# Optimization experiments

Hardware: AMD Instinct MI355X
Metric: run time of the kernel (lower is better)

## Reference

```python
import jax, jax.numpy as jnp
import numpy as np
from jax import lax

ALPHA = 0.5
KERNEL = 25
NUM_P = 16
SEQ_LEN = 1440
PRED_LEN = 720
DWT_LEN = SEQ_LEN // 2 + 2            # 722 (pytorch_wavelets zero-mode, sym3 filt len 6)
FREQ = int(np.ceil(DWT_LEN / 2 * ALPHA) * 2)  # 362

_DEC_LO = np.array([0.035226291882100656, -0.08544127388224149, -0.13501102001039084,
                    0.4598775021193313, 0.8068915093133388, 0.3326705529509569], np.float32)
_DEC_HI = np.array([-0.3326705529509569, 0.8068915093133388, -0.4598775021193313,
                    -0.13501102001039084, 0.08544127388224149, 0.035226291882100656], np.float32)
DEC_LO, DEC_HI = jnp.asarray(_DEC_LO), jnp.asarray(_DEC_HI)
REC_LO, REC_HI = DEC_LO[::-1], DEC_HI[::-1]


def dwt1(x):
    # pytorch_wavelets DWT1DForward(J=1, mode='zero'): zero-pad then stride-2 true conv with dec filters
    B, C, L = x.shape
    out = (L + 5) // 2
    p = 2 * (out - 1) - L + 6
    xp = jnp.pad(x.reshape(B * C, 1, L), ((0, 0), (0, 0), (p // 2, p - p // 2)))
    ker = jnp.stack([DEC_LO[::-1], DEC_HI[::-1]])[:, None, :]   # (2,1,6); xcorr w/ reversed == conv
    y = lax.conv_general_dilated(xp, ker, (2,), 'VALID', dimension_numbers=('NCH', 'OIH', 'NCH'))
    return y[:, 0].reshape(B, C, out), y[:, 1].reshape(B, C, out)


def iwt1(lo, hi):
    # DWT1DInverse mode='zero': conv_transpose stride 2, padding L-2  ->  dilate + conv, pad 1
    B, C, n = lo.shape
    z = jnp.concatenate([lo.reshape(B * C, 1, n), hi.reshape(B * C, 1, n)], axis=1)
    ker = jnp.stack([REC_LO[::-1], REC_HI[::-1]])[None, :, :]   # (O=1, I=2, 6)
    y = lax.conv_general_dilated(z, ker, (1,), [(1, 1)], lhs_dilation=(2,),
                                 dimension_numbers=('NCH', 'OIH', 'NCH'))
    return y[:, 0].reshape(B, C, 2 * n - 4)


def mov_avg(x, k=KERNEL):
    pooled = lax.reduce_window(x, 0.0, lax.add, (1, 1, k), (1, 1, 1), 'VALID') / k
    return jnp.pad(pooled, ((0, 0), (0, 0), (k // 2, k // 2 - (k + 1) % 2)), mode='edge')


def mov_norm(x):
    mean = lax.stop_gradient(mov_avg(x))
    xc = lax.stop_gradient(x - mean)
    std = lax.stop_gradient(mov_avg(jnp.abs(xc))) + 1e-5
    return xc / std, mean, std


def inst_norm(x):
    mean = lax.stop_gradient(jnp.mean(x, -1, keepdims=True))
    xc = x - mean
    var = jnp.mean((xc - jnp.mean(xc, -1, keepdims=True)) ** 2, -1, keepdims=True)
    return xc / jnp.sqrt(var + 1e-5)


def mean_std_mlp(mean, std, mp, sp, mw1, mw2, sw1, sw2, mpred, spred):
    m_all = jnp.mean(mean, -1, keepdims=True)
    s_all = jnp.mean(std, -1, keepdims=True)
    mr = (mean - m_all) @ mp.T
    sr = (std - s_all) @ sp.T
    mr = jax.nn.relu(mr @ mw1.T) @ mw2.T
    sr = jax.nn.relu(sr @ sw1.T) @ sw2.T
    mean_o = mr @ mpred.T + m_all
    std_o = jax.nn.relu(sr @ spred.T + s_all) + 1e-5
    return mean_o, std_o


def forward(x, latent_w, latent_b, acp, dcp):
    xt = jnp.swapaxes(x, -1, 1)                    # (B, C, L)
    ac0, dc0 = dwt1(xt)                            # (B, C, DWT_LEN)
    ac_n = inst_norm(ac0)
    ac, m_ac, s_ac = mov_norm(ac0)
    dc, m_dc, s_dc = mov_norm(dc0)
    m_ac, s_ac = mean_std_mlp(m_ac, s_ac, *acp)    # MLPs[-1]
    m_dc, s_dc = mean_std_mlp(m_dc, s_dc, *dcp)    # MLPs[0]
    dcF = jnp.fft.fft(dc)
    acF = jnp.fft.fft(ac_n)
    idx = jnp.argsort(-jnp.abs(acF), axis=-1)[..., :FREQ]
    amp = ALPHA * jnp.take_along_axis(acF, idx, -1) + (1.0 - ALPHA) * jnp.take_along_axis(dcF, idx, -1)
    B, C, _ = dcF.shape
    bi = jnp.arange(B)[:, None, None]
    ci = jnp.arange(C)[None, :, None]
    dcF = dcF.at[bi, ci, idx].set(amp)
    dc = jnp.real(jnp.fft.ifft(dcF))
    xr = iwt1(ac, dc)                              # (B, C, SEQ_LEN)
    mean = iwt1(m_ac, m_dc)                        # (B, C, PRED_LEN)
    std = iwt1(s_ac, s_dc)
    xr = xr.reshape(B, C, NUM_P, SEQ_LEN // NUM_P)
    emb = xr @ latent_w.T + latent_b               # (B, C, NUM_P, d_model)
    return emb, mean, std


def setup_inputs() -> dict:
    key = jax.random.key(0)
    B, C = 64, 128
    d_model, d_ff = 512, 1024
    s = 0.02
    names_shapes = [
        ('x', (B, SEQ_LEN, C), 1.0),
        ('latent_w', (d_model, SEQ_LEN // NUM_P), s),
    ]
    for pre in ('ac', 'dc'):
        names_shapes += [
            (pre + '_mean_proj', (d_model, DWT_LEN), s),
            (pre + '_std_proj', (d_model, DWT_LEN), s),
            (pre + '_mean_ffn_w1', (d_ff, d_model), s),
            (pre + '_mean_ffn_w2', (d_model, d_ff), s),
            (pre + '_std_ffn_w1', (d_ff, d_model), s),
            (pre + '_std_ffn_w2', (d_model, d_ff), s),
            (pre + '_mean_pred', (PRED_LEN // 2 + 2, d_model), s),
            (pre + '_std_pred', (PRED_LEN // 2 + 2, d_model), s),
        ]
    keys = jax.random.split(key, len(names_shapes))
    inp = {n: jax.random.normal(k, shp, dtype=jnp.float32) * sc
           for (n, shp, sc), k in zip(names_shapes, keys)}
    inp['latent_b'] = jnp.zeros((d_model,), jnp.float32)
    return inp


def reference(x, latent_w, latent_b,
              ac_mean_proj, ac_std_proj, ac_mean_ffn_w1, ac_mean_ffn_w2,
              ac_std_ffn_w1, ac_std_ffn_w2, ac_mean_pred, ac_std_pred,
              dc_mean_proj, dc_std_proj, dc_mean_ffn_w1, dc_mean_ffn_w2,
              dc_std_ffn_w1, dc_std_ffn_w2, dc_mean_pred, dc_std_pred):
    acp = (ac_mean_proj, ac_std_proj, ac_mean_ffn_w1, ac_mean_ffn_w2,
           ac_std_ffn_w1, ac_std_ffn_w2, ac_mean_pred, ac_std_pred)
    dcp = (dc_mean_proj, dc_std_proj, dc_mean_ffn_w1, dc_mean_ffn_w2,
           dc_std_ffn_w1, dc_std_ffn_w2, dc_mean_pred, dc_std_pred)
    return forward(x, latent_w, latent_b, acp, dcp)
```

## Files before the change

kernel.cpp:

```cpp
#include <hip/hip_runtime.h>
#include <cmath>

#define RTOT 8192
#define NDWT 722
#define KP1  736
#define LSEQ 1440
#define NHEAD 362
#define NFREQ 362

typedef __bf16 bf16x8 __attribute__((ext_vector_type(8)));
typedef float f32x4 __attribute__((ext_vector_type(4)));
typedef float f32x2 __attribute__((ext_vector_type(2)));

__device__ __forceinline__ unsigned short f2bf(float f) {
    unsigned u = __float_as_uint(f);
    u += 0x7fffu + ((u >> 16) & 1u);
    return (unsigned short)(u >> 16);
}
__device__ __forceinline__ float bf2f(unsigned short u) {
    return __uint_as_float(((unsigned)u) << 16);
}

__device__ __forceinline__ void cmac(f32x2& s, f32x2 a, f32x2 w) {
    asm("v_pk_fma_f32 %0, %1, %2, %0 op_sel:[0,0,0] op_sel_hi:[0,1,1]\n\t"
        "v_pk_fma_f32 %0, %1, %2, %0 op_sel:[1,1,0] op_sel_hi:[1,0,1] neg_lo:[0,1,0]"
        : "+v"(s) : "v"(a), "v"(w));
}
__device__ __forceinline__ f32x2 cmul(f32x2 a, f32x2 b) {
    f32x2 r;
    asm("v_pk_mul_f32 %0, %1, %2 op_sel:[0,0] op_sel_hi:[0,1]\n\t"
        "v_pk_fma_f32 %0, %1, %2, %0 op_sel:[1,1,0] op_sel_hi:[1,0,1] neg_lo:[0,1,0]"
        : "=&v"(r) : "v"(a), "v"(b));
    return r;
}

__constant__ float c_lo[6] = {0.035226291882100656f, -0.08544127388224149f, -0.13501102001039084f,
                              0.4598775021193313f, 0.8068915093133388f, 0.3326705529509569f};
__constant__ float c_hi[6] = {-0.3326705529509569f, 0.8068915093133388f, -0.4598775021193313f,
                              -0.13501102001039084f, 0.08544127388224149f, 0.035226291882100656f};

__global__ void wtab_kernel(float2* __restrict__ Wtab) {
    int m = blockIdx.x * blockDim.x + threadIdx.x;
    if (m < NDWT) {
        double ang = -2.0 * 3.141592653589793238462643383279502884 * (double)m / (double)NDWT;
        Wtab[m] = make_float2((float)cos(ang), (float)sin(ang));
    }
}

struct CvtDesc { const float* src; unsigned short* dst; int N, K, Np, Kp; };
struct CvtArgs { CvtDesc d[17]; };
__global__ __launch_bounds__(256) void cvt_all_kernel(CvtArgs a) {
    CvtDesc d = a.d[blockIdx.y];
    int idx = blockIdx.x * 256 + threadIdx.x;
    int tot = d.Np * d.Kp;
    if (idx >= tot) return;
    int r = idx / d.Kp, c = idx - r * d.Kp;
    float v = (r < d.N && c < d.K) ? d.src[(size_t)r * d.K + c] : 0.f;
    d.dst[idx] = f2bf(v);
}

__global__ __launch_bounds__(512) void dwt_kernel(const float* __restrict__ x,
                                                  float* __restrict__ ac0,
                                                  float* __restrict__ dc0) {
    int b = blockIdx.x;
    int c = threadIdx.x;
    int t0 = blockIdx.y * 16 + threadIdx.y * 4;
    for (int i = 0; i < 4; i++) {
        int t = t0 + i;
        if (t >= NDWT) break;
        float slo = 0.f, shi = 0.f;
        #pragma unroll
        for (int j = 0; j < 6; j++) {
            int l = 2 * t + 1 - j;
            float v = (l >= 0 && l < LSEQ) ? x[((size_t)b * LSEQ + l) * 128 + c] : 0.f;
            slo += v * c_lo[j];
            shi += v * c_hi[j];
        }
        size_t o = ((size_t)b * 128 + c) * NDWT + t;
        ac0[o] = slo;
        dc0[o] = shi;
    }
}

__device__ __forceinline__ float blockSum256(float v, float* red) {
    #pragma unroll
    for (int o = 32; o > 0; o >>= 1) v += __shfl_down(v, o, 64);
    int lane = threadIdx.x & 63, wid = threadIdx.x >> 6;
    __syncthreads();
    if (lane == 0) red[wid] = v;
    __syncthreads();
    return red[0] + red[1] + red[2] + red[3];
}

template <bool ABS>
__device__ __forceinline__ void pool25(const float* rowv, float* pool, int tid) {
    int i0 = tid * 3;
    if (i0 < 698) {
        float s25 = 0.f;
        #pragma unroll
        for (int j = 0; j < 25; j++) { float v = rowv[i0 + j]; s25 += ABS ? fabsf(v) : v; }
        pool[i0] = s25 * (1.f / 25.f);
        #pragma unroll
        for (int qq = 1; qq < 3; qq++) {
            int i = i0 + qq;
            if (i < 698) {
                float vin = rowv[i + 24], vout = rowv[i - 1];
                s25 += (ABS ? fabsf(vin) : vin) - (ABS ? fabsf(vout) : vout);
                pool[i] = s25 * (1.f / 25.f);
            }
        }
    }
}

__global__ __launch_bounds__(256) void rowstats_kernel(
    const float* __restrict__ ac0in, const float* __restrict__ dc0in,
    float* __restrict__ acn,
    float* __restrict__ acp,
    float* __restrict__ dcp,
    unsigned short* __restrict__ cent,
    float* __restrict__ stat ) {
    __shared__ float row[NDWT];
    __shared__ float xc[NDWT];
    __shared__ float pool[698];
    __shared__ float red[4];
    const int r = blockIdx.x, tid = threadIdx.x;
    const size_t base = (size_t)r * NDWT;
    const size_t baseP = (size_t)r * KP1;
    const size_t CS = (size_t)RTOT * KP1;

    if (blockIdx.y == 0) {
        for (int i = tid; i < NDWT; i += 256) row[i] = ac0in[base + i];
        __syncthreads();
        float s = 0.f;
        for (int i = tid; i < NDWT; i += 256) s += row[i];
        float mean = blockSum256(s, red) * (1.f / 722.f);
        s = 0.f;
        for (int i = tid; i < NDWT; i += 256) s += row[i] - mean;
        float m2 = blockSum256(s, red) * (1.f / 722.f);
        s = 0.f;
        for (int i = tid; i < NDWT; i += 256) { float d = row[i] - mean - m2; s += d * d; }
        float var = blockSum256(s, red) * (1.f / 722.f);
        float inv = 1.f / sqrtf(var + 1e-5f);
        for (int i = tid; i < NDWT; i += 256) acn[base + i] = (row[i] - mean) * inv;

        pool25<false>(row, pool, tid);
        __syncthreads();
        float msum = 0.f;
        for (int l = tid; l < NDWT; l += 256) {
            int pi = l - 12; pi = pi < 0 ? 0 : (pi > 697 ? 697 : pi);
            float m = pool[pi];
            msum += m;
            xc[l] = row[l] - m;
        }
        float m_all = blockSum256(msum, red) * (1.f / 722.f);
        __syncthreads();
        pool25<true>(xc, pool, tid);
        __syncthreads();
        float ssum = 0.f;
        for (int l = tid; l < NDWT; l += 256) {
            int pi = l - 12; pi = pi < 0 ? 0 : (pi > 697 ? 697 : pi);
            float sd = pool[pi] + 1e-5f;
            ssum += sd;
            acp[base + l] = xc[l] / sd;
        }
        float s_all = blockSum256(ssum, red) * (1.f / 722.f);
        if (tid == 0) { stat[r] = m_all; stat[RTOT + r] = s_all; }
        for (int l = tid; l < KP1; l += 256) {
            if (l < NDWT) {
                float m = row[l] - xc[l];
                int pi = l - 12; pi = pi < 0 ? 0 : (pi > 697 ? 697 : pi);
                float sd = pool[pi] + 1e-5f;
                cent[baseP + l]      = f2bf(m - m_all);
                cent[CS + baseP + l] = f2bf(sd - s_all);
            } else { cent[baseP + l] = 0; cent[CS + baseP + l] = 0; }
        }
    } else {
        for (int i = tid; i < NDWT; i += 256) row[i] = dc0in[base + i];
        __syncthreads();
        pool25<false>(row, pool, tid);
        __syncthreads();
        float msum2 = 0.f;
        for (int l = tid; l < NDWT; l += 256) {
            int pi = l - 12; pi = pi < 0 ? 0 : (pi > 697 ? 697 : pi);
            float m = pool[pi];
            msum2 += m;
            xc[l] = row[l] - m;
        }
        float m_all2 = blockSum256(msum2, red) * (1.f / 722.f);
        __syncthreads();
        pool25<true>(xc, pool, tid);
        __syncthreads();
        float ssum2 = 0.f;
        for (int l = tid; l < NDWT; l += 256) {
            int pi = l - 12; pi = pi < 0 ? 0 : (pi > 697 ? 697 : pi);
            float sd = pool[pi] + 1e-5f;
            ssum2 += sd;
            dcp[base + l] = xc[l] / sd;
        }
        float s_all2 = blockSum256(ssum2, red) * (1.f / 722.f);
        if (tid == 0) { stat[2 * RTOT + r] = m_all2; stat[3 * RTOT + r] = s_all2; }
        for (int l = tid; l < KP1; l += 256) {
            if (l < NDWT) {
                float m = row[l] - xc[l];
                int pi = l - 12; pi = pi < 0 ? 0 : (pi > 697 ? 697 : pi);
                float sd = pool[pi] + 1e-5f;
                cent[2 * CS + baseP + l] = f2bf(m - m_all2);
                cent[3 * CS + baseP + l] = f2bf(sd - s_all2);
            } else { cent[2 * CS + baseP + l] = 0; cent[3 * CS + baseP + l] = 0; }
        }
    }
}

__device__ void fft722_dev(f32x2* X, f32x2* T, const f32x2* Wt, const f32x2* W19) {
    const int tid = threadIdx.x;
    if (tid < 190) {
        const int c = tid / 38;
        const int g = tid - c * 38;
        const int p = (g >= 19) ? 1 : 0;
        const int rr = g - 19 * p;
        const int t0 = c * 4;
        const int nt = (c == 4) ? 3 : 4;
        const f32x2* xp = X + 2 * rr + p;
        f32x2 st[4], w[4], s[4];
        #pragma unroll
        for (int i = 0; i < 4; i++) {
            int ti = t0 + i; if (ti > 18) ti = 0;
            st[i] = W19[ti];
            w[i] = f32x2{1.f, 0.f};
            s[i] = f32x2{0.f, 0.f};
        }
        for (int j = 0; j < 19; j++) {
            f32x2 a = xp[38 * j];
            #pragma unroll
            for (int i = 0; i < 4; i++) { cmac(s[i], a, w[i]); w[i] = cmul(w[i], st[i]); }
        }
        f32x2* Tp = T + p * 361 + rr * 19 + t0;
        #pragma unroll
        for (int i = 0; i < 4; i++) if (i < nt) Tp[i] = s[i];
    }
    __syncthreads();
    if (tid < 190) {
        const int c = tid / 38;
        const int g = tid - c * 38;
        const int p = (g >= 19) ? 1 : 0;
        const int t = g - 19 * p;
        const int j0 = c * 4;
        const int nj = (c == 4) ? 3 : 4;
        const f32x2* Tp = T + p * 361 + t;
        int kk[4];
        f32x2 st[4], w[4], s[4];
        #pragma unroll
        for (int i = 0; i < 4; i++) {
            int jj = j0 + i;
            kk[i] = (jj > 18) ? 0 : (t + 19 * jj);
            st[i] = Wt[2 * kk[i]];
            w[i] = f32x2{1.f, 0.f};
            s[i] = f32x2{0.f, 0.f};
        }
        for (int rr = 0; rr < 19; rr++) {
            f32x2 a = Tp[19 * rr];
            #pragma unroll
            for (int i = 0; i < 4; i++) { cmac(s[i], a, w[i]); w[i] = cmul(w[i], st[i]); }
        }
        f32x2* Xp = X + p * 361;
        #pragma unroll
        for (int i = 0; i < 4; i++) if (i < nj) Xp[kk[i]] = s[i];
    }
    __syncthreads();
    for (int k = tid; k < 361; k += 256) {
        f32x2 e = X[k], o = X[361 + k], w = Wt[k];
        f32x2 tt = {0.f, 0.f};
        cmac(tt, o, w);
        X[k] = e + tt;
        X[361 + k] = e - tt;
    }
    __syncthreads();
}

__global__ __launch_bounds__(256) void fft_mix_kernel(const float* __restrict__ acn,
                                                      float* __restrict__ dcp,
                                                      const f32x2* __restrict__ Wtab) {
    __shared__ f32x2 Wt[NDWT];
    __shared__ f32x2 W19s[19];
    __shared__ f32x2 B1[NDWT];
    __shared__ f32x2 B2[NDWT];
    __shared__ float smag[NDWT];
    __shared__ unsigned hist[256];
    __shared__ unsigned suf[256];
    __shared__ unsigned sh_digit, sh_rem;
    const int r = blockIdx.x, tid = threadIdx.x;
    const size_t base = (size_t)r * NDWT;

    for (int i = tid; i < NDWT; i += 256) Wt[i] = Wtab[i];
    if (tid < 19) W19s[tid] = Wtab[38 * tid];
    for (int i = tid; i < NDWT; i += 256) B1[i] = f32x2{acn[base + i], dcp[base + i]};
    __syncthreads();
    fft722_dev(B1, B2, Wt, W19s);
    for (int k = tid; k < 362; k += 256) {
        int m = (NDWT - k) % NDWT;
        f32x2 zk = B1[k], zm = B1[m];
        f32x2 ak = {0.5f * (zk.x + zm.x), 0.5f * (zk.y - zm.y)};
        f32x2 dk = {0.5f * (zk.y + zm.y), 0.5f * (zm.x - zk.x)};
        B1[k] = ak; B2[k] = dk;
        smag[k] = ak.x * ak.x + ak.y * ak.y;
        if (m != k) {
            f32x2 am = {0.5f * (zm.x + zk.x), 0.5f * (zm.y - zk.y)};
            f32x2 dm = {0.5f * (zm.y + zk.y), 0.5f * (zk.x - zm.x)};
            B1[m] = am; B2[m] = dm;
            smag[m] = am.x * am.x + am.y * am.y;
        }
    }
    __syncthreads();

    unsigned prefix = 0, rem = NFREQ;
    for (int shift = 24; shift >= 0; shift -= 8) {
        hist[tid] = 0;
        __syncthreads();
        unsigned hm = (shift == 24) ? 0u : (0xFFFFFFFFu << (shift + 8));
        for (int i = tid; i < NDWT; i += 256) {
            unsigned b = __float_as_uint(smag[i]);
            if ((b & hm) == prefix) atomicAdd(&hist[(b >> shift) & 255], 1u);
        }
        __syncthreads();
        suf[tid] = hist[tid];
        __syncthreads();
        for (int off = 1; off < 256; off <<= 1) {
            unsigned v = (tid + off < 256) ? suf[tid + off] : 0;
            __syncthreads();
            suf[tid] += v;
            __syncthreads();
        }
        unsigned Shere = suf[tid];
        unsigned Snext = (tid < 255) ? suf[tid + 1] : 0;
        if (Shere >= rem && Snext < rem) { sh_digit = (unsigned)tid; sh_rem = rem - Snext; }
        __syncthreads();
        prefix |= (sh_digit << shift);
        rem = sh_rem;
        __syncthreads();
    }
    int c0 = tid * 3, cnt = 0;
    #pragma unroll
    for (int j = 0; j < 3; j++) {
        int i = c0 + j;
        if (i < NDWT && __float_as_uint(smag[i]) == prefix) cnt++;
    }
    suf[tid] = (unsigned)cnt;
    __syncthreads();
    for (int off = 1; off < 256; off <<= 1) {
        unsigned v = (tid >= off) ? suf[tid - off] : 0;
        __syncthreads();
        suf[tid] += v;
        __syncthreads();
    }
    int myexc = (int)suf[tid] - cnt, o = 0;
    #pragma unroll
    for (int j = 0; j < 3; j++) {
        int i = c0 + j;
        if (i < NDWT) {
            unsigned b = __float_as_uint(smag[i]);
            int f = (b > prefix) ? 1 : 0;
            if (b == prefix) { if ((unsigned)(myexc + o) < rem) f = 1; o++; }
            smag[i] = f ? 1.f : 0.f;
        }
    }
    __syncthreads();

    for (int i = tid; i < NDWT; i += 256) {
        f32x2 d = B2[i];
        if (smag[i] != 0.f) { f32x2 a = B1[i]; d.x = 0.5f * (a.x + d.x); d.y = 0.5f * (a.y + d.y); }
        B1[i] = f32x2{d.x, -d.y};
    }
    __syncthreads();
    fft722_dev(B1, B2, Wt, W19s);
    for (int i = tid; i < NDWT; i += 256) dcp[base + i] = B1[i].x * (1.f / 722.f);
}

__global__ __launch_bounds__(256) void iwt_heads_kernel(const unsigned short* __restrict__ heads,
                                                        float* __restrict__ out_mean,
                                                        float* __restrict__ out_std) {
    const int z = blockIdx.z;
    const int r = blockIdx.x;
    const int t = blockIdx.y * 256 + threadIdx.x;
    if (t >= 720) return;
    const size_t HR = (size_t)RTOT * NHEAD;
    const unsigned short* lp = heads + (size_t)z * HR + (size_t)r * NHEAD;
    const unsigned short* hp = heads + (size_t)(2 + z) * HR + (size_t)r * NHEAD;
    float* out = (z ? out_std : out_mean) + (size_t)r * 720;
    float s = 0.f;
    if (t & 1) {
        int j0 = (t - 1) >> 1;
        #pragma unroll
        for (int i = 0; i < 3; i++) s += bf2f(lp[j0 + i]) * c_lo[2 * i] + bf2f(hp[j0 + i]) * c_hi[2 * i];
    } else {
        int j0 = t >> 1;
        #pragma unroll
        for (int i = 0; i < 3; i++) s += bf2f(lp[j0 + i]) * c_lo[2 * i + 1] + bf2f(hp[j0 + i]) * c_hi[2 * i + 1];
    }
    out[t] = s;
}

__global__ __launch_bounds__(256) void iwt_xr_kernel(const float* __restrict__ lo,
                                                     const float* __restrict__ hi,
                                                     unsigned short* __restrict__ xrbf) {
    const int r = blockIdx.x;
    const int t = blockIdx.y * 256 + threadIdx.x;
    if (blockIdx.y == 0 && threadIdx.x < 96) {
        int sub = threadIdx.x / 6, c = 90 + threadIdx.x % 6;
        xrbf[((size_t)r * 16 + sub) * 96 + c] = 0;
    }
    if (t >= LSEQ) return;
    const float* lp = lo + (size_t)r * NDWT;
    const float* hp = hi + (size_t)r * NDWT;
    float s = 0.f;
    if (t & 1) {
        int j0 = (t - 1) >> 1;
        #pragma unroll
        for (int i = 0; i < 3; i++) s += lp[j0 + i] * c_lo[2 * i] + hp[j0 + i] * c_hi[2 * i];
    } else {
        int j0 = t >> 1;
        #pragma unroll
        for (int i = 0; i < 3; i++) s += lp[j0 + i] * c_lo[2 * i + 1] + hp[j0 + i] * c_hi[2 * i + 1];
    }
    xrbf[((size_t)r * 16 + t / 90) * 96 + (t % 90)] = f2bf(s);
}

struct ZPtrs { const unsigned short* p[4]; };
template <int EPI>
__global__ __launch_bounds__(256) void mfma_gemm_z(
    const unsigned short* __restrict__ A, int lda, size_t zsA,
    ZPtrs Wz, int ldw,
    void* __restrict__ Cout, int ldc, size_t zsC, int Nc,
    const float* __restrict__ biasBase, const float* __restrict__ cbias,
    int Ksteps) {
    __shared__ unsigned short As[2][128 * 32];
    __shared__ unsigned short Bs[2][128 * 32];
    const int z = blockIdx.z;
    const unsigned short* Az = A + (size_t)z * zsA;
    const unsigned short* W = Wz.p[z];
    const int tid = threadIdx.x;
    const int lane = tid & 63, wid = tid >> 6;
    const int bm = blockIdx.x * 128, bn = blockIdx.y * 128;
    const int wr = (wid >> 1) * 64, wc = (wid & 1) * 64;
    f32x4 acc[4][4] = {};
    const int srow = (lane >> 2);
    const int scol = (lane & 3) * 8;
    const int ch0 = wid * 2, ch1 = wid * 2 + 1;
    const unsigned short* ga0 = Az + (size_t)(bm + ch0 * 16 + srow) * lda + scol;
    const unsigned short* ga1 = Az + (size_t)(bm + ch1 * 16 + srow) * lda + scol;
    const unsigned short* gb0 = W + (size_t)(bn + ch0 * 16 + srow) * ldw + scol;
    const unsigned short* gb1 = W + (size_t)(bn + ch1 * 16 + srow) * ldw + scol;

#define STAGE_GL(buf, ks) do { const int k0_ = (ks) * 32;                                      \
    __builtin_amdgcn_global_load_lds((const __attribute__((address_space(1))) unsigned int*)(ga0 + k0_), \
        (__attribute__((address_space(3))) unsigned int*)(&As[buf][ch0 * 512]), 16, 0, 0);     \
    __builtin_amdgcn_global_load_lds((const __attribute__((address_space(1))) unsigned int*)(gb0 + k0_), \
        (__attribute__((address_space(3))) unsigned int*)(&Bs[buf][ch0 * 512]), 16, 0, 0);     \
    __builtin_amdgcn_global_load_lds((const __attribute__((address_space(1))) unsigned int*)(ga1 + k0_), \
        (__attribute__((address_space(3))) unsigned int*)(&As[buf][ch1 * 512]), 16, 0, 0);     \
    __builtin_amdgcn_global_load_lds((const __attribute__((address_space(1))) unsigned int*)(gb1 + k0_), \
        (__attribute__((address_space(3))) unsigned int*)(&Bs[buf][ch1 * 512]), 16, 0, 0);     \
    } while (0)

    STAGE_GL(0, 0);
    __syncthreads();
    int cur = 0;
    const int kof = (lane >> 4) * 8;
    for (int ks = 0; ks < Ksteps; ks++) {
        if (ks + 1 < Ksteps) STAGE_GL(cur ^ 1, ks + 1);
        bf16x8 af[4], bfr[4];
        #pragma unroll
        for (int m = 0; m < 4; m++)
            af[m] = *reinterpret_cast<const bf16x8*>(&As[cur][(wr + m * 16 + (lane & 15)) * 32 + kof]);
        #pragma unroll
        for (int n = 0; n < 4; n++)
            bfr[n] = *reinterpret_cast<const bf16x8*>(&Bs[cur][(wc + n * 16 + (lane & 15)) * 32 + kof]);
        #pragma unroll
        for (int m = 0; m < 4; m++)
            #pragma unroll
            for (int n = 0; n < 4; n++)
                acc[m][n] = __builtin_amdgcn_mfma_f32_16x16x32_bf16(af[m], bfr[n], acc[m][n], 0, 0, 0);
        __syncthreads();
        cur ^= 1;
    }
#undef STAGE_GL

    unsigned short* Cb = (unsigned short*)Cout + (size_t)z * zsC;
    float* Cf = (float*)Cout + (size_t)z * zsC;
    const int crow0 = bm + wr + (lane >> 4) * 4;
    const int ccol0 = bn + wc + (lane & 15);
    #pragma unroll
    for (int m = 0; m < 4; m++) {
        #pragma unroll
        for (int n = 0; n < 4; n++) {
            const int col = ccol0 + n * 16;
            if (col < Nc) {
                #pragma unroll
                for (int q = 0; q < 4; q++) {
                    const int row = crow0 + m * 16 + q;
                    float v = acc[m][n][q];
                    if (EPI == 0) {
                        Cb[(size_t)row * ldc + col] = f2bf(v);
                    } else if (EPI == 1) {
                        Cb[(size_t)row * ldc + col] = f2bf(fmaxf(v, 0.f));
                    } else if (EPI == 4) {
                        Cf[(size_t)row * ldc + col] = v + cbias[col];
                    } else {
                        float ob = biasBase[(size_t)z * RTOT + row];
                        if (z & 1) v = fmaxf(v + ob, 0.f) + 1e-5f;
                        else       v += ob;
                        Cb[(size_t)row * ldc + col] = f2bf(v);
                    }
                }
            }
        }
    }
}

extern "C" void kernel_launch(void* const* d_in, const int* in_sizes, int n_in,
                              void* d_out, int out_size, void* d_ws, size_t ws_size,
                              hipStream_t stream) {
    const float* x = (const float*)d_in[0];
    const float* latent_w = (const float*)d_in[1];
    int p0;
    const float* latent_b;
    if (n_in > 2 && in_sizes[2] == 512) { latent_b = (const float*)d_in[2]; p0 = 3; }
    else                                { latent_b = (const float*)d_in[18]; p0 = 2; }

    char* wp = (char*)d_ws;
    auto alloc = [&](size_t bytes) { char* p = wp; wp += (bytes + 255) & ~(size_t)255; return p; };
    const size_t RN = (size_t)RTOT * NDWT;
    float* acn  = (float*)alloc(RN * 4);
    float* dcb  = (float*)alloc(RN * 4);
    float* acp  = (float*)alloc(RN * 4);
    float* stat = (float*)alloc(4 * RTOT * 4);
    float2* Wtab = (float2*)alloc(NDWT * 8);
    unsigned short* cent  = (unsigned short*)alloc((size_t)4 * RTOT * KP1 * 2);
    unsigned short* mlpB4 = (unsigned short*)alloc((size_t)4 * RTOT * 512 * 2);
    unsigned short* mlpA4 = (unsigned short*)alloc((size_t)4 * RTOT * 1024 * 2);
    unsigned short* mlpC4 = (unsigned short*)alloc((size_t)4 * RTOT * 512 * 2);
    unsigned short* heads = mlpB4;
    unsigned short* xrbf = mlpC4;
    unsigned short *projW[4], *w1W[4], *w2W[4], *predW[4];
    for (int z = 0; z < 4; z++) {
        projW[z] = (unsigned short*)alloc((size_t)512 * KP1 * 2);
        w1W[z]   = (unsigned short*)alloc((size_t)1024 * 512 * 2);
        w2W[z]   = (unsigned short*)alloc((size_t)512 * 1024 * 2);
        predW[z] = (unsigned short*)alloc((size_t)384 * 512 * 2);
    }
    unsigned short* latwb = (unsigned short*)alloc((size_t)512 * 96 * 2);
    (void)ws_size;

    CvtArgs ca;
    int si = 0;
    for (int z = 0; z < 4; z++) {
        int branch = z >> 1, isStd = z & 1, wb = p0 + branch * 8;
        ca.d[si++] = {(const float*)d_in[wb + isStd],         projW[z], 512, NDWT, 512, KP1};
        ca.d[si++] = {(const float*)d_in[wb + 2 + 2 * isStd], w1W[z], 1024, 512, 1024, 512};
        ca.d[si++] = {(const float*)d_in[wb + 3 + 2 * isStd], w2W[z], 512, 1024, 512, 1024};
        ca.d[si++] = {(const float*)d_in[wb + 6 + isStd],     predW[z], NHEAD, 512, 384, 512};
    }
    ca.d[16] = {latent_w, latwb, 512, 90, 512, 96};
    cvt_all_kernel<<<dim3(2048, 17), dim3(256), 0, stream>>>(ca);

    wtab_kernel<<<dim3(3), dim3(256), 0, stream>>>(Wtab);
    dwt_kernel<<<dim3(64, 46), dim3(128, 4), 0, stream>>>(x, acn, dcb);
    rowstats_kernel<<<dim3(RTOT, 2), dim3(256), 0, stream>>>(acn, dcb, acn, acp, dcb, cent, stat);
    fft_mix_kernel<<<dim3(RTOT), dim3(256), 0, stream>>>(acn, dcb, (const f32x2*)Wtab);

    ZPtrs Zp = {{projW[0], projW[1], projW[2], projW[3]}};
    ZPtrs Z1 = {{w1W[0], w1W[1], w1W[2], w1W[3]}};
    ZPtrs Z2 = {{w2W[0], w2W[1], w2W[2], w2W[3]}};
    ZPtrs Zh = {{predW[0], predW[1], predW[2], predW[3]}};
    mfma_gemm_z<0><<<dim3(64, 4, 4), dim3(256), 0, stream>>>(
        cent, KP1, (size_t)RTOT * KP1, Zp, KP1, mlpB4, 512, (size_t)RTOT * 512, 512, nullptr, nullptr, KP1 / 32);
    mfma_gemm_z<1><<<dim3(64, 8, 4), dim3(256), 0, stream>>>(
        mlpB4, 512, (size_t)RTOT * 512, Z1, 512, mlpA4, 1024, (size_t)RTOT * 1024, 1024, nullptr, nullptr, 16);
    mfma_gemm_z<0><<<dim3(64, 4, 4), dim3(256), 0, stream>>>(
        mlpA4, 1024, (size_t)RTOT * 1024, Z2, 1024, mlpC4, 512, (size_t)RTOT * 512, 512, nullptr, nullptr, 32);
    mfma_gemm_z<5><<<dim3(64, 3, 4), dim3(256), 0, stream>>>(
        mlpC4, 512, (size_t)RTOT * 512, Zh, 512, heads, NHEAD, (size_t)RTOT * NHEAD, NHEAD, stat, nullptr, 16);

    float* out = (float*)d_out;
    float* out_mean = out + (size_t)67108864;
    float* out_std  = out_mean + (size_t)5898240;
    iwt_heads_kernel<<<dim3(RTOT, 3, 2), dim3(256), 0, stream>>>(heads, out_mean, out_std);
    iwt_xr_kernel<<<dim3(RTOT, 6), dim3(256), 0, stream>>>(acp, dcb, xrbf);

    ZPtrs Zl = {{latwb, latwb, latwb, latwb}};
    mfma_gemm_z<4><<<dim3(1024, 4, 1), dim3(256), 0, stream>>>(
        xrbf, 96, 0, Zl, 96, out, 512, 0, 512, nullptr, latent_b, 3);
}
```

Before: 615.9 us.

## Tile DWT through LDS for coalesced stores; use explicit vmcnt waits in GEMM loop

The DWT kernel now stages a 68x128 input tile in shared memory using float4 loads. Each thread then computes along time for a fixed channel, so the writes into the channel-major (b,c,t) outputs are coalesced along t, where before they were strided. The GEMM main loop replaces __syncthreads with explicit s_waitcnt vmcnt counters plus raw s_barrier, so the next stage's global-to-LDS loads can stay in flight while the current tile is consumed. The hand-written waitcnt logic depends on the exact count of outstanding loads per stage (four), and getting it wrong would be a correctness risk.

```diff
diff --git a/kernel.cpp b/kernel.cpp
--- a/kernel.cpp
+++ b/kernel.cpp
@@ -59,26 +59,42 @@
     d.dst[idx] = f2bf(v);
 }
 
-__global__ __launch_bounds__(512) void dwt_kernel(const float* __restrict__ x,
+__global__ __launch_bounds__(256) void dwt_kernel(const float* __restrict__ x,
                                                   float* __restrict__ ac0,
                                                   float* __restrict__ dc0) {
-    int b = blockIdx.x;
-    int c = threadIdx.x;
-    int t0 = blockIdx.y * 16 + threadIdx.y * 4;
-    for (int i = 0; i < 4; i++) {
-        int t = t0 + i;
-        if (t >= NDWT) break;
-        float slo = 0.f, shi = 0.f;
-        #pragma unroll
-        for (int j = 0; j < 6; j++) {
-            int l = 2 * t + 1 - j;
-            float v = (l >= 0 && l < LSEQ) ? x[((size_t)b * LSEQ + l) * 128 + c] : 0.f;
-            slo += v * c_lo[j];
-            shi += v * c_hi[j];
-        }
-        size_t o = ((size_t)b * 128 + c) * NDWT + t;
-        ac0[o] = slo;
-        dc0[o] = shi;
+    __shared__ float xs[68][129];
+    const int b = blockIdx.x;
+    const int t0 = blockIdx.y * 32;
+    const int tid = threadIdx.x;
+    const int lbase = 2 * t0 - 4;
+    for (int i = tid; i < 68 * 32; i += 256) {
+        int ri = i >> 5;
+        int c4 = (i & 31) * 4;
+        int l = lbase + ri;
+        float4 v = make_float4(0.f, 0.f, 0.f, 0.f);
+        if (l >= 0 && l < LSEQ)
+            v = *reinterpret_cast<const float4*>(&x[((size_t)b * LSEQ + l) * 128 + c4]);
+        xs[ri][c4] = v.x; xs[ri][c4 + 1] = v.y; xs[ri][c4 + 2] = v.z; xs[ri][c4 + 3] = v.w;
+    }
+    __syncthreads();
+    const int tt = tid & 31;
+    const int t = t0 + tt;
+    const int cw = tid >> 5;
+    if (t < NDWT) {
+        #pragma unroll 4
+        for (int co = 0; co < 16; co++) {
+            int c = co * 8 + cw;
+            float slo = 0.f, shi = 0.f;
+            #pragma unroll
+            for (int j = 0; j < 6; j++) {
+                float v = xs[2 * tt + 5 - j][c];
+                slo += v * c_lo[j];
+                shi += v * c_hi[j];
+            }
+            size_t o = ((size_t)b * 128 + c) * NDWT + t;
+            ac0[o] = slo;
+            dc0[o] = shi;
+        }
     }
 }
 
@@ -462,11 +478,17 @@
     } while (0)
 
     STAGE_GL(0, 0);
-    __syncthreads();
     int cur = 0;
     const int kof = (lane >> 4) * 8;
     for (int ks = 0; ks < Ksteps; ks++) {
-        if (ks + 1 < Ksteps) STAGE_GL(cur ^ 1, ks + 1);
+        if (ks + 1 < Ksteps) {
+            STAGE_GL(cur ^ 1, ks + 1);
+            asm volatile("s_waitcnt vmcnt(4)" ::: "memory");
+        } else {
+            asm volatile("s_waitcnt vmcnt(0)" ::: "memory");
+        }
+        __builtin_amdgcn_s_barrier();
+        __builtin_amdgcn_sched_barrier(0);
         bf16x8 af[4], bfr[4];
         #pragma unroll
         for (int m = 0; m < 4; m++)
@@ -479,7 +501,8 @@
             #pragma unroll
             for (int n = 0; n < 4; n++)
                 acc[m][n] = __builtin_amdgcn_mfma_f32_16x16x32_bf16(af[m], bfr[n], acc[m][n], 0, 0, 0);
-        __syncthreads();
+        __builtin_amdgcn_s_barrier();
+        __builtin_amdgcn_sched_barrier(0);
         cur ^= 1;
     }
 #undef STAGE_GL
@@ -563,7 +586,7 @@
     cvt_all_kernel<<<dim3(2048, 17), dim3(256), 0, stream>>>(ca);
 
     wtab_kernel<<<dim3(3), dim3(256), 0, stream>>>(Wtab);
-    dwt_kernel<<<dim3(64, 46), dim3(128, 4), 0, stream>>>(x, acn, dcb);
+    dwt_kernel<<<dim3(64, 23), dim3(256), 0, stream>>>(x, acn, dcb);
     rowstats_kernel<<<dim3(RTOT, 2), dim3(256), 0, stream>>>(acn, dcb, acn, acp, dcb, cent, stat);
     fft_mix_kernel<<<dim3(RTOT), dim3(256), 0, stream>>>(acn, dcb, (const f32x2*)Wtab);
 
```

Measured after the change: 539.3 us. 1.14x faster.
